# Kernel tuning notes

Hardware: AMD Instinct MI355X
Metric: run time of the kernel (lower is better)

## Reference

```python
import jax, jax.numpy as jnp
import numpy as np
import math

D = 128      # d_model == num_filters
L = 4        # num_conv_layers
K = 7        # kernel_size
H = 8        # num_heads
B, S = 64, 400


def setup_inputs() -> dict:
    key = jax.random.key(0)
    ks = jax.random.split(key, 24)
    s = 0.02
    inp = {}
    inp['x'] = jax.random.normal(ks[0], (B, S, D), dtype=jnp.float32)
    # per-conv-layer params (stacked over L)
    inp['ln_g'] = jnp.ones((L, D), jnp.float32)
    inp['ln_b'] = jnp.zeros((L, D), jnp.float32)
    inp['dw_w'] = jax.random.normal(ks[1], (L, D, D, K), dtype=jnp.float32) * s
    inp['dw_b'] = jnp.zeros((L, D), jnp.float32)
    inp['pw_w'] = jax.random.normal(ks[2], (L, D, D), dtype=jnp.float32) * s
    inp['pw_b'] = jnp.zeros((L, D), jnp.float32)
    # attention block
    inp['attln_g'] = jnp.ones((D,), jnp.float32)
    inp['attln_b'] = jnp.zeros((D,), jnp.float32)
    inp['wq'] = jax.random.normal(ks[3], (D, D), dtype=jnp.float32) * s
    inp['bq'] = jnp.zeros((D,), jnp.float32)
    inp['wk'] = jax.random.normal(ks[4], (D, D), dtype=jnp.float32) * s
    inp['bk'] = jnp.zeros((D,), jnp.float32)
    inp['wv'] = jax.random.normal(ks[5], (D, D), dtype=jnp.float32) * s
    inp['bv'] = jnp.zeros((D,), jnp.float32)
    inp['wp'] = jax.random.normal(ks[6], (D, D), dtype=jnp.float32) * s
    inp['bp'] = jnp.zeros((D,), jnp.float32)
    # ffn
    inp['ffnln_g'] = jnp.ones((D,), jnp.float32)
    inp['ffnln_b'] = jnp.zeros((D,), jnp.float32)
    inp['fc_w'] = jax.random.normal(ks[7], (D, D), dtype=jnp.float32) * s
    inp['fc_b'] = jnp.zeros((D,), jnp.float32)
    return inp


def _layernorm(x, g, b, eps=1e-5):
    mu = jnp.mean(x, axis=-1, keepdims=True)
    var = jnp.var(x, axis=-1, keepdims=True)
    return (x - mu) * jax.lax.rsqrt(var + eps) * g + b


def _pos_encoding(seq_len, channels, dtype):
    pos = jnp.arange(seq_len, dtype=dtype)                       # [S]
    freq = 1.0 / (10000.0 ** (jnp.arange(0, channels, 2, dtype=dtype) / channels))
    sin_inp = pos[:, None] * freq[None, :]                       # [S, C/2]
    return jnp.concatenate([jnp.sin(sin_inp), jnp.cos(sin_inp)], axis=-1)  # [S, C]


def _encoder_fwd(x, ln_g, ln_b, dw_w, dw_b, pw_w, pw_b,
                 attln_g, attln_b, wq, bq, wk, bk, wv, bv, wp, bp,
                 ffnln_g, ffnln_b, fc_w, fc_b):
    b, s, d = x.shape
    out = x + _pos_encoding(s, d, x.dtype)[None, :, :]

    # conv stack: LN -> transpose -> (full) conv K -> pointwise conv -> transpose
    pad = dw_w.shape[-1] // 2
    for i in range(dw_w.shape[0]):
        h = _layernorm(out, ln_g[i], ln_b[i])
        t = jnp.transpose(h, (0, 2, 1))                          # [B, D, S]
        t = jax.lax.conv_general_dilated(
            t, dw_w[i], window_strides=(1,), padding=[(pad, pad)],
            dimension_numbers=('NCH', 'OIH', 'NCH')) + dw_b[i][None, :, None]
        t = jnp.einsum('bds,fd->bfs', t, pw_w[i]) + pw_b[i][None, :, None]
        out = jnp.transpose(t, (0, 2, 1))                        # [B, S, D]

    # causal self-attention (explicit scores, per original)
    h = _layernorm(out, attln_g, attln_b)
    hd = d // H
    q = (jnp.einsum('bsd,od->bso', h, wq) + bq).reshape(b, s, H, hd)
    k = (jnp.einsum('bsd,od->bso', h, wk) + bk).reshape(b, s, H, hd)
    v = (jnp.einsum('bsd,od->bso', h, wv) + bv).reshape(b, s, H, hd)
    att = jnp.einsum('bqhd,bkhd->bhqk', q, k) / math.sqrt(hd)    # [B, H, S, S]
    causal = jnp.tril(jnp.ones((s, s), dtype=bool))
    att = jnp.where(causal[None, None], att, jnp.asarray(-1e10, att.dtype))
    att = jax.nn.softmax(att, axis=-1)
    y = jnp.einsum('bhqk,bkhd->bqhd', att, v).reshape(b, s, d)
    y = jnp.einsum('bsd,od->bso', y, wp) + bp

    # ffn
    y = _layernorm(y, ffnln_g, ffnln_b)
    y = jnp.einsum('bsd,od->bso', y, fc_w) + fc_b
    return jax.nn.relu(y)


def reference(x, ln_g, ln_b, dw_w, dw_b, pw_w, pw_b,
              attln_g, attln_b, wq, bq, wk, bk, wv, bv, wp, bp,
              ffnln_g, ffnln_b, fc_w, fc_b):
    return _encoder_fwd(x, ln_g, ln_b, dw_w, dw_b, pw_w, pw_b,
                        attln_g, attln_b, wq, bq, wk, bk, wv, bv, wp, bp,
                        ffnln_g, ffnln_b, fc_w, fc_b)
```

## Files before the change

### kernel.cpp

```cpp
#include <hip/hip_runtime.h>
#include <hip/hip_bf16.h>
#include <math.h>

#define Dm 128
#define Lc 4
#define Kc 7
#define Hh 8
#define Bb 64
#define Ss 400
#define SsP 416
#define TOK (Bb*Ss)

typedef __attribute__((ext_vector_type(8))) short bf16x8;
typedef __attribute__((ext_vector_type(4))) float f32x4;

__device__ __forceinline__ unsigned short f2bf(float f) {
    __hip_bfloat16 h = __float2bfloat16(f);
    return __builtin_bit_cast(unsigned short, h);
}
__device__ __forceinline__ unsigned int packbf(float a, float b) {
    return (unsigned int)f2bf(a) | ((unsigned int)f2bf(b) << 16);
}
__device__ __forceinline__ bf16x8 pack8(float4 a, float4 b) {
    unsigned int u0 = packbf(a.x, a.y), u1 = packbf(a.z, a.w);
    unsigned int u2 = packbf(b.x, b.y), u3 = packbf(b.z, b.w);
    uint4 u = make_uint4(u0, u1, u2, u3);
    return __builtin_bit_cast(bf16x8, u);
}


__global__ __launch_bounds__(256) void prep_misc(const float* __restrict__ wq, const float* __restrict__ wk,
                                                 const float* __restrict__ wv, const float* __restrict__ wp,
                                                 const float* __restrict__ fc,
                                                 const float* __restrict__ pw_w, const float* __restrict__ dw_b,
                                                 const float* __restrict__ pw_b,
                                                 float* __restrict__ pe, unsigned short* __restrict__ wf,
                                                 float* __restrict__ mb) {
    int blk = blockIdx.x;
    if (blk < 200) {
        int s = blk * 2 + (threadIdx.x >> 7);
        int c = threadIdx.x & 127;
        int j = (c < 64) ? c : (c - 64);
        float freq = expf(-(2.0f * j / 128.0f) * 9.210340371976184f);
        float a = (float)s * freq;
        pe[s * Dm + c] = (c < 64) ? sinf(a) : cosf(a);
    } else if (blk < 520) {
        int idx = (blk - 200) * 256 + threadIdx.x;
        int m = idx >> 14;
        int r = idx & 16383;
        int fragi = r >> 9, lr = (r >> 3) & 63, j = r & 7;
        int kb = fragi >> 3, nb = fragi & 7;
        int o = nb * 16 + (lr & 15);
        int d = kb * 32 + (lr >> 4) * 8 + j;
        const float* src = (m == 0) ? wq : (m == 1) ? wk : (m == 2) ? wv : (m == 3) ? wp : fc;
        wf[idx] = f2bf(src[o * Dm + d]);
    } else {
        int l = blk - 520;
        int f = threadIdx.x;
        if (f < Dm) {
            const float* pwl = pw_w + ((size_t)l * Dm + f) * Dm;
            const float* db  = dw_b + l * Dm;
            float acc = pw_b[l * Dm + f];
            #pragma unroll 8
            for (int c4 = 0; c4 < 32; ++c4) {
                float4 p = *(const float4*)(pwl + c4 * 4);
                float4 d = *(const float4*)(db + c4 * 4);
                acc += p.x * d.x + p.y * d.y + p.z * d.z + p.w * d.w;
            }
            mb[l * Dm + f] = acc;
        }
    }
}


__global__ __launch_bounds__(256) void merge_conv_mfma(const float* __restrict__ pw_w,
                                                       const float* __restrict__ dw_w,
                                                       unsigned short* __restrict__ mwf) {
    __shared__ unsigned short dwS[64][136];
    int blk = blockIdx.x;
    int ih = blk & 1;
    int k  = (blk >> 1) % 7;
    int l  = blk / 14;
    int tid = threadIdx.x, lane = tid & 63, w = tid >> 6;

    const float* dwl = dw_w + (size_t)l * (Dm * Dm * Kc) + k;
    for (int it = 0; it < 32; ++it) {
        int idx = it * 256 + tid;
        int c = idx >> 6, il = idx & 63;
        int i = ih * 64 + il;
        dwS[il][c] = f2bf(dwl[(size_t)(c * Dm + i) * Kc]);
    }
    __syncthreads();

    const float* pwl = pw_w + (size_t)l * Dm * Dm;
    int arow = lane & 15, ac = (lane >> 4) * 8;
    f32x4 acc[2][4];
    #pragma unroll
    for (int n = 0; n < 2; ++n)
        #pragma unroll
        for (int m = 0; m < 4; ++m) acc[n][m] = (f32x4){0.f, 0.f, 0.f, 0.f};

    #pragma unroll
    for (int kb = 0; kb < 4; ++kb) {
        int c0 = kb * 32 + ac;
        bf16x8 Bf[2];
        #pragma unroll
        for (int n = 0; n < 2; ++n) {
            int f = (w * 2 + n) * 16 + arow;
            const float* rp = pwl + (size_t)f * Dm + c0;
            Bf[n] = pack8(*(const float4*)rp, *(const float4*)(rp + 4));
        }
        #pragma unroll
        for (int m = 0; m < 4; ++m) {
            bf16x8 af = *(const bf16x8*)&dwS[m * 16 + arow][c0];
            acc[0][m] = __builtin_amdgcn_mfma_f32_16x16x32_bf16(af, Bf[0], acc[0][m], 0, 0, 0);
            acc[1][m] = __builtin_amdgcn_mfma_f32_16x16x32_bf16(af, Bf[1], acc[1][m], 0, 0, 0);
        }
    }
    #pragma unroll
    for (int n = 0; n < 2; ++n) {
        int nb = w * 2 + n;
        #pragma unroll
        for (int m = 0; m < 4; ++m) {
            int i0 = ih * 64 + m * 16 + (lane >> 4) * 4;
            int ib = i0 >> 5, i32 = i0 & 31;
            int lanep = ((i32 >> 3) << 4) | arow;
            int jb = i32 & 7;
            size_t frag = ((size_t)(l * 28 + (k * 4 + ib)) * 8 + nb);
            *(uint2*)(mwf + frag * 512 + lanep * 8 + jb) =
                make_uint2(packbf(acc[n][m][0], acc[n][m][1]),
                           packbf(acc[n][m][2], acc[n][m][3]));
        }
    }
}


__device__ __forceinline__ uint4 ln_pack(float4 v0, float4 v1,
                                         const float* __restrict__ g,
                                         const float* __restrict__ b, int c16) {
    float sum = v0.x + v0.y + v0.z + v0.w + v1.x + v1.y + v1.z + v1.w;
    float sq  = v0.x*v0.x + v0.y*v0.y + v0.z*v0.z + v0.w*v0.w
              + v1.x*v1.x + v1.y*v1.y + v1.z*v1.z + v1.w*v1.w;
    #pragma unroll
    for (int off = 8; off; off >>= 1) {
        sum += __shfl_xor(sum, off);
        sq  += __shfl_xor(sq, off);
    }
    float mu = sum * (1.0f / 128.0f);
    float var = sq * (1.0f / 128.0f) - mu * mu;
    float rs = rsqrtf(var + 1e-5f);
    float4 g0 = *(const float4*)(g + c16 * 8);
    float4 g1 = *(const float4*)(g + c16 * 8 + 4);
    float4 b0 = *(const float4*)(b + c16 * 8);
    float4 b1 = *(const float4*)(b + c16 * 8 + 4);
    uint4 o;
    o.x = packbf((v0.x - mu) * rs * g0.x + b0.x, (v0.y - mu) * rs * g0.y + b0.y);
    o.y = packbf((v0.z - mu) * rs * g0.z + b0.z, (v0.w - mu) * rs * g0.w + b0.w);
    o.z = packbf((v1.x - mu) * rs * g1.x + b1.x, (v1.y - mu) * rs * g1.y + b1.y);
    o.w = packbf((v1.z - mu) * rs * g1.z + b1.z, (v1.w - mu) * rs * g1.w + b1.w);
    return o;
}


__global__ __launch_bounds__(256) void conv_mfma(const float* __restrict__ in,
                                                 const float* __restrict__ pe,
                                                 const unsigned short* __restrict__ mwf,
                                                 const float* __restrict__ mb,
                                                 const float* __restrict__ lng,
                                                 const float* __restrict__ lnb,
                                                 float* __restrict__ out) {
    __shared__ unsigned short hs[54][136];
    int tid = threadIdx.x;
    int lane = tid & 63, w = tid >> 6;
    int bI = blockIdx.x / 9;
    int st = blockIdx.x % 9;
    int s0 = st * 48;
    const float* ib = in + (size_t)bI * Ss * Dm;
    for (int c = tid; c < 54 * 16; c += 256) {
        int row = c >> 4, c16 = c & 15;
        int gs = s0 - 3 + row;
        if (gs >= 0 && gs < Ss) {
            const float* rp = ib + (size_t)gs * Dm + c16 * 8;
            float4 v0 = *(const float4*)rp;
            float4 v1 = *(const float4*)(rp + 4);
            if (pe) {
                const float* pp = pe + (size_t)gs * Dm + c16 * 8;
                float4 p0 = *(const float4*)pp;
                float4 p1 = *(const float4*)(pp + 4);
                v0.x += p0.x; v0.y += p0.y; v0.z += p0.z; v0.w += p0.w;
                v1.x += p1.x; v1.y += p1.y; v1.z += p1.z; v1.w += p1.w;
            }
            *(uint4*)&hs[row][c16 * 8] = ln_pack(v0, v1, lng, lnb, c16);
        } else {
            *(uint4*)&hs[row][c16 * 8] = make_uint4(0u, 0u, 0u, 0u);
        }
    }
    __syncthreads();

    f32x4 acc[2][3];
    #pragma unroll
    for (int n = 0; n < 2; ++n)
        #pragma unroll
        for (int m = 0; m < 3; ++m) acc[n][m] = (f32x4){0.f, 0.f, 0.f, 0.f};

    int nb0 = w * 2;
    int arow = lane & 15, acol = (lane >> 4) * 8;
    #pragma unroll 4
    for (int kb = 0; kb < 28; ++kb) {
        int k = kb >> 2, i0 = (kb & 3) * 32;
        bf16x8 b0 = *(const bf16x8*)(mwf + ((size_t)(kb * 8 + nb0)) * 512 + lane * 8);
        bf16x8 b1 = *(const bf16x8*)(mwf + ((size_t)(kb * 8 + nb0 + 1)) * 512 + lane * 8);
        #pragma unroll
        for (int m = 0; m < 3; ++m) {
            bf16x8 af = *(const bf16x8*)&hs[m * 16 + arow + k][i0 + acol];
            acc[0][m] = __builtin_amdgcn_mfma_f32_16x16x32_bf16(af, b0, acc[0][m], 0, 0, 0);
            acc[1][m] = __builtin_amdgcn_mfma_f32_16x16x32_bf16(af, b1, acc[1][m], 0, 0, 0);
        }
    }
    int rr = (lane >> 4) * 4;
    #pragma unroll
    for (int n = 0; n < 2; ++n) {
        int f0 = (nb0 + n) * 16;
        float bias = mb[f0 + arow];
        #pragma unroll
        for (int m = 0; m < 3; ++m)
            #pragma unroll
            for (int r = 0; r < 4; ++r) {
                int s = s0 + m * 16 + rr + r;
                if (s < Ss)
                    out[((size_t)bI * Ss + s) * Dm + f0 + arow] = acc[n][m][r] + bias;
            }
    }
}


__global__ __launch_bounds__(256) void qkv_mfma(const float* __restrict__ in,
                                                const float* __restrict__ lng,
                                                const float* __restrict__ lnb,
                                                const unsigned short* __restrict__ wfb,
                                                const float* __restrict__ bq,
                                                const float* __restrict__ bk,
                                                const float* __restrict__ bv,
                                                unsigned short* __restrict__ Qo,
                                                unsigned short* __restrict__ Ko,
                                                unsigned short* __restrict__ Vo) {
    __shared__ unsigned short hs[80][136];
    int tid = threadIdx.x;
    int lane = tid & 63, w = tid >> 6;
    int mat = blockIdx.y;
    int bI = blockIdx.x / 5;
    int sb = (blockIdx.x % 5) * 80;
    const float* ib = in + ((size_t)bI * Ss + sb) * Dm;
    for (int c = tid; c < 80 * 16; c += 256) {
        int row = c >> 4, c16 = c & 15;
        const float* rp = ib + (size_t)row * Dm + c16 * 8;
        float4 v0 = *(const float4*)rp;
        float4 v1 = *(const float4*)(rp + 4);
        *(uint4*)&hs[row][c16 * 8] = ln_pack(v0, v1, lng, lnb, c16);
    }
    __syncthreads();

    const unsigned short* wf = wfb + (size_t)mat * 16384;
    f32x4 acc[2][5];
    #pragma unroll
    for (int n = 0; n < 2; ++n)
        #pragma unroll
        for (int m = 0; m < 5; ++m) acc[n][m] = (f32x4){0.f, 0.f, 0.f, 0.f};

    int nb0 = w * 2;
    int arow = lane & 15, acol = (lane >> 4) * 8;
    #pragma unroll
    for (int kb = 0; kb < 4; ++kb) {
        bf16x8 b0 = *(const bf16x8*)(wf + ((size_t)(kb * 8 + nb0)) * 512 + lane * 8);
        bf16x8 b1 = *(const bf16x8*)(wf + ((size_t)(kb * 8 + nb0 + 1)) * 512 + lane * 8);
        #pragma unroll
        for (int m = 0; m < 5; ++m) {
            bf16x8 af = *(const bf16x8*)&hs[m * 16 + arow][kb * 32 + acol];
            acc[0][m] = __builtin_amdgcn_mfma_f32_16x16x32_bf16(af, b0, acc[0][m], 0, 0, 0);
            acc[1][m] = __builtin_amdgcn_mfma_f32_16x16x32_bf16(af, b1, acc[1][m], 0, 0, 0);
        }
    }
    int rr = (lane >> 4) * 4;
    const float* bias = (mat == 0) ? bq : (mat == 1) ? bk : bv;
    float sc = (mat == 0) ? 0.25f : 1.0f;
    #pragma unroll
    for (int n = 0; n < 2; ++n) {
        int hI = nb0 + n;
        float bvv = bias[hI * 16 + arow];
        if (mat < 2) {
            unsigned short* qo = (mat == 0) ? Qo : Ko;
            #pragma unroll
            for (int m = 0; m < 5; ++m)
                #pragma unroll
                for (int r = 0; r < 4; ++r) {
                    int s = sb + m * 16 + rr + r;
                    qo[(((size_t)(bI * Hh + hI)) * Ss + s) * 16 + arow] = f2bf((acc[n][m][r] + bvv) * sc);
                }
        } else {
            unsigned short* base = Vo + ((size_t)(bI * Hh + hI) * 16 + arow) * SsP + sb;
            #pragma unroll
            for (int m = 0; m < 5; ++m) {
                unsigned lo = packbf(acc[n][m][0] + bvv, acc[n][m][1] + bvv);
                unsigned hi = packbf(acc[n][m][2] + bvv, acc[n][m][3] + bvv);
                *(uint2*)(base + m * 16 + rr) = make_uint2(lo, hi);
            }
        }
    }
}


__global__ __launch_bounds__(256) void gemm2(const void* __restrict__ inv,
                                             const unsigned short* __restrict__ wf,
                                             const float* __restrict__ bias,
                                             const float* __restrict__ lng,
                                             const float* __restrict__ lnb,
                                             float* __restrict__ out, int relu) {
    __shared__ unsigned short hs[80][136];
    int tid = threadIdx.x;
    int lane = tid & 63, w = tid >> 6;
    size_t tok0 = (size_t)blockIdx.x * 80;
    if (lng) {
        const float* ib = (const float*)inv + tok0 * Dm;
        for (int c = tid; c < 80 * 16; c += 256) {
            int row = c >> 4, c16 = c & 15;
            const float* rp = ib + (size_t)row * Dm + c16 * 8;
            float4 v0 = *(const float4*)rp;
            float4 v1 = *(const float4*)(rp + 4);
            *(uint4*)&hs[row][c16 * 8] = ln_pack(v0, v1, lng, lnb, c16);
        }
    } else {
        const unsigned short* ib = (const unsigned short*)inv + tok0 * Dm;
        for (int c = tid; c < 80 * 16; c += 256) {
            int row = c >> 4, c16 = c & 15;
            *(uint4*)&hs[row][c16 * 8] = *(const uint4*)(ib + (size_t)row * Dm + c16 * 8);
        }
    }
    __syncthreads();

    f32x4 acc[2][5];
    #pragma unroll
    for (int n = 0; n < 2; ++n)
        #pragma unroll
        for (int m = 0; m < 5; ++m) acc[n][m] = (f32x4){0.f, 0.f, 0.f, 0.f};

    int nb0 = w * 2;
    int arow = lane & 15, acol = (lane >> 4) * 8;
    #pragma unroll
    for (int kb = 0; kb < 4; ++kb) {
        bf16x8 b0 = *(const bf16x8*)(wf + ((size_t)(kb * 8 + nb0)) * 512 + lane * 8);
        bf16x8 b1 = *(const bf16x8*)(wf + ((size_t)(kb * 8 + nb0 + 1)) * 512 + lane * 8);
        #pragma unroll
        for (int m = 0; m < 5; ++m) {
            bf16x8 af = *(const bf16x8*)&hs[m * 16 + arow][kb * 32 + acol];
            acc[0][m] = __builtin_amdgcn_mfma_f32_16x16x32_bf16(af, b0, acc[0][m], 0, 0, 0);
            acc[1][m] = __builtin_amdgcn_mfma_f32_16x16x32_bf16(af, b1, acc[1][m], 0, 0, 0);
        }
    }
    int rr = (lane >> 4) * 4;
    #pragma unroll
    for (int n = 0; n < 2; ++n) {
        int f0 = (nb0 + n) * 16;
        float bvv = bias[f0 + arow];
        #pragma unroll
        for (int m = 0; m < 5; ++m)
            #pragma unroll
            for (int r = 0; r < 4; ++r) {
                float v = acc[n][m][r] + bvv;
                if (relu) v = fmaxf(v, 0.f);
                out[(tok0 + m * 16 + rr + r) * Dm + f0 + arow] = v;
            }
    }
}


__global__ __launch_bounds__(256) void attn_mfma(const unsigned short* __restrict__ Q,
                                                 const unsigned short* __restrict__ Kb,
                                                 const unsigned short* __restrict__ VT,
                                                 unsigned short* __restrict__ out) {
    int wid = threadIdx.x >> 6, lane = threadIdx.x & 63;
    int gw = blockIdx.x * 4 + wid;
    int bh = gw & 511, qt = gw >> 9;
    int q15 = lane & 15, h = lane >> 4;
    int qg = qt * 16 + q15;

    uint4 qv = make_uint4(0u, 0u, 0u, 0u);
    if (h < 2) qv = *(const uint4*)(Q + ((size_t)bh * Ss + qg) * 16 + h * 8);
    bf16x8 qf = __builtin_bit_cast(bf16x8, qv);

    f32x4 o = (f32x4){0.f, 0.f, 0.f, 0.f};
    float mrow = -1e30f, lrow = 0.f;
    const unsigned short* kbase = Kb + (size_t)bh * Ss * 16;
    const unsigned short* vbase = VT + ((size_t)bh * 16 + q15) * SsP;

    for (int kt = 0; kt <= qt; kt += 2) {
        int kg0 = kt * 16 + q15;
        uint4 k0 = make_uint4(0u, 0u, 0u, 0u), k1 = make_uint4(0u, 0u, 0u, 0u);
        if (h < 2) {
            k0 = *(const uint4*)(kbase + (size_t)kg0 * 16 + h * 8);
            if (kg0 + 16 < Ss)
                k1 = *(const uint4*)(kbase + (size_t)(kg0 + 16) * 16 + h * 8);
        }
        f32x4 z = (f32x4){0.f, 0.f, 0.f, 0.f};
        f32x4 s0 = __builtin_amdgcn_mfma_f32_16x16x32_bf16(__builtin_bit_cast(bf16x8, k0), qf, z, 0, 0, 0);
        f32x4 s1 = __builtin_amdgcn_mfma_f32_16x16x32_bf16(__builtin_bit_cast(bf16x8, k1), qf, z, 0, 0, 0);

        float p[8];
        #pragma unroll
        for (int r = 0; r < 4; ++r) {
            int ka = kt * 16 + h * 4 + r;
            p[r]     = (ka <= qg)      ? s0[r] : -1e30f;
            p[r + 4] = (ka + 16 <= qg) ? s1[r] : -1e30f;
        }
        float tm = fmaxf(fmaxf(fmaxf(p[0], p[1]), fmaxf(p[2], p[3])),
                         fmaxf(fmaxf(p[4], p[5]), fmaxf(p[6], p[7])));
        tm = fmaxf(tm, __shfl_xor(tm, 16));
        tm = fmaxf(tm, __shfl_xor(tm, 32));
        float mnew = fmaxf(mrow, tm);
        float corr = __expf(mrow - mnew);
        float psum = 0.f;
        #pragma unroll
        for (int r = 0; r < 8; ++r) { p[r] = __expf(p[r] - mnew); psum += p[r]; }
        psum += __shfl_xor(psum, 16);
        psum += __shfl_xor(psum, 32);
        lrow = lrow * corr + psum;
        mrow = mnew;
        o[0] *= corr; o[1] *= corr; o[2] *= corr; o[3] *= corr;

        unsigned pk0 = packbf(p[0], p[1]), pk1 = packbf(p[2], p[3]);
        unsigned pk2 = packbf(p[4], p[5]), pk3 = packbf(p[6], p[7]);
        int srcA = q15 + ((h & 1) << 5);
        int srcB = srcA + 16;
        unsigned a0 = __shfl(pk0, srcA), a1 = __shfl(pk1, srcA);
        unsigned a2 = __shfl(pk0, srcB), a3 = __shfl(pk1, srcB);
        unsigned b0 = __shfl(pk2, srcA), b1 = __shfl(pk3, srcA);
        unsigned b2 = __shfl(pk2, srcB), b3 = __shfl(pk3, srcB);
        bool t1 = h >= 2;
        uint4 pw = make_uint4(t1 ? b0 : a0, t1 ? b1 : a1, t1 ? b2 : a2, t1 ? b3 : a3);

        uint4 vv = *(const uint4*)(vbase + kt * 16 + h * 8);
        o = __builtin_amdgcn_mfma_f32_16x16x32_bf16(__builtin_bit_cast(bf16x8, vv),
                                                    __builtin_bit_cast(bf16x8, pw), o, 0, 0, 0);
    }
    float inv = 1.0f / lrow;
    int bI = bh >> 3, hh = bh & 7;
    unsigned short* op = out + ((size_t)bI * Ss + qg) * Dm + hh * 16 + h * 4;
    *(uint2*)op = make_uint2(packbf(o[0] * inv, o[1] * inv),
                             packbf(o[2] * inv, o[3] * inv));
}


extern "C" void kernel_launch(void* const* d_in, const int* in_sizes, int n_in,
                              void* d_out, int out_size, void* d_ws, size_t ws_size,
                              hipStream_t stream) {
    (void)in_sizes; (void)n_in; (void)out_size; (void)ws_size;
    const float* x       = (const float*)d_in[0];
    const float* ln_g    = (const float*)d_in[1];
    const float* ln_b    = (const float*)d_in[2];
    const float* dw_w    = (const float*)d_in[3];
    const float* dw_b    = (const float*)d_in[4];
    const float* pw_w    = (const float*)d_in[5];
    const float* pw_b    = (const float*)d_in[6];
    const float* attln_g = (const float*)d_in[7];
    const float* attln_b = (const float*)d_in[8];
    const float* wq = (const float*)d_in[9];
    const float* bq = (const float*)d_in[10];
    const float* wk = (const float*)d_in[11];
    const float* bk = (const float*)d_in[12];
    const float* wv = (const float*)d_in[13];
    const float* bv = (const float*)d_in[14];
    const float* wp = (const float*)d_in[15];
    const float* bp = (const float*)d_in[16];
    const float* ffnln_g = (const float*)d_in[17];
    const float* ffnln_b = (const float*)d_in[18];
    const float* fc_w = (const float*)d_in[19];
    const float* fc_b = (const float*)d_in[20];

    float* ws = (float*)d_ws;
    float* pe = ws;
    float* mb = pe + 51200;
    float* C1 = mb + 512;
    float* C2 = C1 + 3276800;
    unsigned short* mwf = (unsigned short*)(C2 + 3276800);
    unsigned short* wfb = mwf + 458752;
    unsigned short* Qb  = wfb + 81920;
    unsigned short* Kb2 = Qb + 3276800;
    unsigned short* VTb = Kb2 + 3276800;
    unsigned short* A1b = VTb + 3407872;

    prep_misc<<<524, 256, 0, stream>>>(wq, wk, wv, wp, fc_w, pw_w, dw_b, pw_b, pe, wfb, mb);
    merge_conv_mfma<<<56, 256, 0, stream>>>(pw_w, dw_w, mwf);

    conv_mfma<<<Bb * 9, 256, 0, stream>>>(x,  pe,      mwf,                    mb,           ln_g,           ln_b,           C1);
    conv_mfma<<<Bb * 9, 256, 0, stream>>>(C1, nullptr, mwf + 114688,           mb + Dm,      ln_g + Dm,      ln_b + Dm,      C2);
    conv_mfma<<<Bb * 9, 256, 0, stream>>>(C2, nullptr, mwf + 2 * 114688,       mb + 2 * Dm,  ln_g + 2 * Dm,  ln_b + 2 * Dm,  C1);
    conv_mfma<<<Bb * 9, 256, 0, stream>>>(C1, nullptr, mwf + 3 * 114688,       mb + 3 * Dm,  ln_g + 3 * Dm,  ln_b + 3 * Dm,  C2);

    qkv_mfma<<<dim3(320, 3), 256, 0, stream>>>(C2, attln_g, attln_b, wfb, bq, bk, bv, Qb, Kb2, VTb);
    attn_mfma<<<3200, 256, 0, stream>>>(Qb, Kb2, VTb, A1b);
    gemm2<<<320, 256, 0, stream>>>(A1b, wfb + 3 * 16384, bp, nullptr, nullptr, C1, 0);

    gemm2<<<320, 256, 0, stream>>>(C1, wfb + 4 * 16384, fc_b, ffnln_g, ffnln_b, (float*)d_out, 1);
}
```

Baseline: 130.1 us.

## Merge prep kernels, split-bf16 conv weight merge, fuse QK in qkv, widen attention tile

Folds the conv weight-merge kernel into the prep kernel so one launch does both. The merge now uses a hi/lo bf16 split with three MFMAs for better weight precision. qkv now runs two grid rows, with one block computing both Q and K to reuse the layernormed tile. The attention inner loop handles four key tiles per online-softmax step, with V padded to 448 so the extra reads stay in bounds. This cuts launches, reductions and rescale work per key, at the cost of more registers, extra merge MFMAs and fewer qkv blocks.

```diff
diff --git a/kernel.cpp b/kernel.cpp
--- a/kernel.cpp
+++ b/kernel.cpp
@@ -8,12 +8,15 @@
 #define Hh 8
 #define Bb 64
 #define Ss 400
-#define SsP 416
+#define SsP 448
 #define TOK (Bb*Ss)
 
 typedef __attribute__((ext_vector_type(8))) short bf16x8;
 typedef __attribute__((ext_vector_type(4))) float f32x4;
 
+__device__ __forceinline__ float bf2f(unsigned int u) {
+    union { unsigned int i; float f; } x; x.i = u << 16; return x.f;
+}
 __device__ __forceinline__ unsigned short f2bf(float f) {
     __hip_bfloat16 h = __float2bfloat16(f);
     return __builtin_bit_cast(unsigned short, h);
@@ -21,31 +24,30 @@
 __device__ __forceinline__ unsigned int packbf(float a, float b) {
     return (unsigned int)f2bf(a) | ((unsigned int)f2bf(b) << 16);
 }
-__device__ __forceinline__ bf16x8 pack8(float4 a, float4 b) {
-    unsigned int u0 = packbf(a.x, a.y), u1 = packbf(a.z, a.w);
-    unsigned int u2 = packbf(b.x, b.y), u3 = packbf(b.z, b.w);
-    uint4 u = make_uint4(u0, u1, u2, u3);
-    return __builtin_bit_cast(bf16x8, u);
-}
-
-
-__global__ __launch_bounds__(256) void prep_misc(const float* __restrict__ wq, const float* __restrict__ wk,
-                                                 const float* __restrict__ wv, const float* __restrict__ wp,
-                                                 const float* __restrict__ fc,
-                                                 const float* __restrict__ pw_w, const float* __restrict__ dw_b,
-                                                 const float* __restrict__ pw_b,
-                                                 float* __restrict__ pe, unsigned short* __restrict__ wf,
-                                                 float* __restrict__ mb) {
+
+
+__global__ __launch_bounds__(256) void prep_all(const float* __restrict__ wq, const float* __restrict__ wk,
+                                                const float* __restrict__ wv, const float* __restrict__ wp,
+                                                const float* __restrict__ fc,
+                                                const float* __restrict__ pw_w, const float* __restrict__ dw_w,
+                                                const float* __restrict__ dw_b, const float* __restrict__ pw_b,
+                                                float* __restrict__ pe, unsigned short* __restrict__ wf,
+                                                float* __restrict__ mb, unsigned short* __restrict__ mwf) {
+    __shared__ unsigned short hiS[64][136];
+    __shared__ unsigned short loS[64][136];
     int blk = blockIdx.x;
+    int tid = threadIdx.x;
     if (blk < 200) {
-        int s = blk * 2 + (threadIdx.x >> 7);
-        int c = threadIdx.x & 127;
+        int s = blk * 2 + (tid >> 7);
+        int c = tid & 127;
         int j = (c < 64) ? c : (c - 64);
         float freq = expf(-(2.0f * j / 128.0f) * 9.210340371976184f);
         float a = (float)s * freq;
         pe[s * Dm + c] = (c < 64) ? sinf(a) : cosf(a);
-    } else if (blk < 520) {
-        int idx = (blk - 200) * 256 + threadIdx.x;
+        return;
+    }
+    if (blk < 520) {
+        int idx = (blk - 200) * 256 + tid;
         int m = idx >> 14;
         int r = idx & 16383;
         int fragi = r >> 9, lr = (r >> 3) & 63, j = r & 7;
@@ -54,9 +56,11 @@
         int d = kb * 32 + (lr >> 4) * 8 + j;
         const float* src = (m == 0) ? wq : (m == 1) ? wk : (m == 2) ? wv : (m == 3) ? wp : fc;
         wf[idx] = f2bf(src[o * Dm + d]);
-    } else {
+        return;
+    }
+    if (blk < 524) {
         int l = blk - 520;
-        int f = threadIdx.x;
+        int f = tid;
         if (f < Dm) {
             const float* pwl = pw_w + ((size_t)l * Dm + f) * Dm;
             const float* db  = dw_b + l * Dm;
@@ -69,26 +73,24 @@
             }
             mb[l * Dm + f] = acc;
         }
-    }
-}
-
-
-__global__ __launch_bounds__(256) void merge_conv_mfma(const float* __restrict__ pw_w,
-                                                       const float* __restrict__ dw_w,
-                                                       unsigned short* __restrict__ mwf) {
-    __shared__ unsigned short dwS[64][136];
-    int blk = blockIdx.x;
-    int ih = blk & 1;
-    int k  = (blk >> 1) % 7;
-    int l  = blk / 14;
-    int tid = threadIdx.x, lane = tid & 63, w = tid >> 6;
+        return;
+    }
+    int mblk = blk - 524;
+    int ih = mblk & 1;
+    int k  = (mblk >> 1) % 7;
+    int l  = mblk / 14;
+    int lane = tid & 63, w = tid >> 6;
 
     const float* dwl = dw_w + (size_t)l * (Dm * Dm * Kc) + k;
     for (int it = 0; it < 32; ++it) {
         int idx = it * 256 + tid;
         int c = idx >> 6, il = idx & 63;
         int i = ih * 64 + il;
-        dwS[il][c] = f2bf(dwl[(size_t)(c * Dm + i) * Kc]);
+        float x = dwl[(size_t)(c * Dm + i) * Kc];
+        unsigned short hi = f2bf(x);
+        float lo = x - bf2f(hi);
+        hiS[il][c] = hi;
+        loS[il][c] = f2bf(lo);
     }
     __syncthreads();
 
@@ -103,18 +105,41 @@
     #pragma unroll
     for (int kb = 0; kb < 4; ++kb) {
         int c0 = kb * 32 + ac;
-        bf16x8 Bf[2];
+        bf16x8 Bhi[2], Blo[2];
         #pragma unroll
         for (int n = 0; n < 2; ++n) {
             int f = (w * 2 + n) * 16 + arow;
             const float* rp = pwl + (size_t)f * Dm + c0;
-            Bf[n] = pack8(*(const float4*)rp, *(const float4*)(rp + 4));
+            float4 a = *(const float4*)rp;
+            float4 b = *(const float4*)(rp + 4);
+            float v[8] = {a.x, a.y, a.z, a.w, b.x, b.y, b.z, b.w};
+            unsigned short hh[8], ll[8];
+            #pragma unroll
+            for (int j = 0; j < 8; ++j) {
+                hh[j] = f2bf(v[j]);
+                ll[j] = f2bf(v[j] - bf2f(hh[j]));
+            }
+            uint4 uh = make_uint4((unsigned)hh[0] | ((unsigned)hh[1] << 16),
+                                  (unsigned)hh[2] | ((unsigned)hh[3] << 16),
+                                  (unsigned)hh[4] | ((unsigned)hh[5] << 16),
+                                  (unsigned)hh[6] | ((unsigned)hh[7] << 16));
+            uint4 ul = make_uint4((unsigned)ll[0] | ((unsigned)ll[1] << 16),
+                                  (unsigned)ll[2] | ((unsigned)ll[3] << 16),
+                                  (unsigned)ll[4] | ((unsigned)ll[5] << 16),
+                                  (unsigned)ll[6] | ((unsigned)ll[7] << 16));
+            Bhi[n] = __builtin_bit_cast(bf16x8, uh);
+            Blo[n] = __builtin_bit_cast(bf16x8, ul);
         }
         #pragma unroll
         for (int m = 0; m < 4; ++m) {
-            bf16x8 af = *(const bf16x8*)&dwS[m * 16 + arow][c0];
-            acc[0][m] = __builtin_amdgcn_mfma_f32_16x16x32_bf16(af, Bf[0], acc[0][m], 0, 0, 0);
-            acc[1][m] = __builtin_amdgcn_mfma_f32_16x16x32_bf16(af, Bf[1], acc[1][m], 0, 0, 0);
+            bf16x8 ahi = *(const bf16x8*)&hiS[m * 16 + arow][c0];
+            bf16x8 alo = *(const bf16x8*)&loS[m * 16 + arow][c0];
+            #pragma unroll
+            for (int n = 0; n < 2; ++n) {
+                acc[n][m] = __builtin_amdgcn_mfma_f32_16x16x32_bf16(ahi, Bhi[n], acc[n][m], 0, 0, 0);
+                acc[n][m] = __builtin_amdgcn_mfma_f32_16x16x32_bf16(ahi, Blo[n], acc[n][m], 0, 0, 0);
+                acc[n][m] = __builtin_amdgcn_mfma_f32_16x16x32_bf16(alo, Bhi[n], acc[n][m], 0, 0, 0);
+            }
         }
     }
     #pragma unroll
@@ -247,7 +272,7 @@
     __shared__ unsigned short hs[80][136];
     int tid = threadIdx.x;
     int lane = tid & 63, w = tid >> 6;
-    int mat = blockIdx.y;
+    int y = blockIdx.y;
     int bI = blockIdx.x / 5;
     int sb = (blockIdx.x % 5) * 80;
     const float* ib = in + ((size_t)bI * Ss + sb) * Dm;
@@ -260,49 +285,52 @@
     }
     __syncthreads();
 
-    const unsigned short* wf = wfb + (size_t)mat * 16384;
-    f32x4 acc[2][5];
-    #pragma unroll
-    for (int n = 0; n < 2; ++n)
-        #pragma unroll
-        for (int m = 0; m < 5; ++m) acc[n][m] = (f32x4){0.f, 0.f, 0.f, 0.f};
-
     int nb0 = w * 2;
     int arow = lane & 15, acol = (lane >> 4) * 8;
-    #pragma unroll
-    for (int kb = 0; kb < 4; ++kb) {
-        bf16x8 b0 = *(const bf16x8*)(wf + ((size_t)(kb * 8 + nb0)) * 512 + lane * 8);
-        bf16x8 b1 = *(const bf16x8*)(wf + ((size_t)(kb * 8 + nb0 + 1)) * 512 + lane * 8);
-        #pragma unroll
-        for (int m = 0; m < 5; ++m) {
-            bf16x8 af = *(const bf16x8*)&hs[m * 16 + arow][kb * 32 + acol];
-            acc[0][m] = __builtin_amdgcn_mfma_f32_16x16x32_bf16(af, b0, acc[0][m], 0, 0, 0);
-            acc[1][m] = __builtin_amdgcn_mfma_f32_16x16x32_bf16(af, b1, acc[1][m], 0, 0, 0);
-        }
-    }
-    int rr = (lane >> 4) * 4;
-    const float* bias = (mat == 0) ? bq : (mat == 1) ? bk : bv;
-    float sc = (mat == 0) ? 0.25f : 1.0f;
-    #pragma unroll
-    for (int n = 0; n < 2; ++n) {
-        int hI = nb0 + n;
-        float bvv = bias[hI * 16 + arow];
-        if (mat < 2) {
-            unsigned short* qo = (mat == 0) ? Qo : Ko;
-            #pragma unroll
-            for (int m = 0; m < 5; ++m)
+    int nmat = (y == 0) ? 2 : 1;
+    for (int mi = 0; mi < nmat; ++mi) {
+        int mat = (y == 0) ? mi : 2;
+        const unsigned short* wf = wfb + (size_t)mat * 16384;
+        f32x4 acc[2][5];
+        #pragma unroll
+        for (int n = 0; n < 2; ++n)
+            #pragma unroll
+            for (int m = 0; m < 5; ++m) acc[n][m] = (f32x4){0.f, 0.f, 0.f, 0.f};
+        #pragma unroll
+        for (int kb = 0; kb < 4; ++kb) {
+            bf16x8 b0 = *(const bf16x8*)(wf + ((size_t)(kb * 8 + nb0)) * 512 + lane * 8);
+            bf16x8 b1 = *(const bf16x8*)(wf + ((size_t)(kb * 8 + nb0 + 1)) * 512 + lane * 8);
+            #pragma unroll
+            for (int m = 0; m < 5; ++m) {
+                bf16x8 af = *(const bf16x8*)&hs[m * 16 + arow][kb * 32 + acol];
+                acc[0][m] = __builtin_amdgcn_mfma_f32_16x16x32_bf16(af, b0, acc[0][m], 0, 0, 0);
+                acc[1][m] = __builtin_amdgcn_mfma_f32_16x16x32_bf16(af, b1, acc[1][m], 0, 0, 0);
+            }
+        }
+        int rr = (lane >> 4) * 4;
+        const float* bias = (mat == 0) ? bq : (mat == 1) ? bk : bv;
+        float sc = (mat == 0) ? 0.25f : 1.0f;
+        #pragma unroll
+        for (int n = 0; n < 2; ++n) {
+            int hI = nb0 + n;
+            float bvv = bias[hI * 16 + arow];
+            if (mat < 2) {
+                unsigned short* qo = (mat == 0) ? Qo : Ko;
                 #pragma unroll
-                for (int r = 0; r < 4; ++r) {
-                    int s = sb + m * 16 + rr + r;
-                    qo[(((size_t)(bI * Hh + hI)) * Ss + s) * 16 + arow] = f2bf((acc[n][m][r] + bvv) * sc);
+                for (int m = 0; m < 5; ++m)
+                    #pragma unroll
+                    for (int r = 0; r < 4; ++r) {
+                        int s = sb + m * 16 + rr + r;
+                        qo[(((size_t)(bI * Hh + hI)) * Ss + s) * 16 + arow] = f2bf((acc[n][m][r] + bvv) * sc);
+                    }
+            } else {
+                unsigned short* base = Vo + ((size_t)(bI * Hh + hI) * 16 + arow) * SsP + sb;
+                #pragma unroll
+                for (int m = 0; m < 5; ++m) {
+                    unsigned lo = packbf(acc[n][m][0] + bvv, acc[n][m][1] + bvv);
+                    unsigned hi = packbf(acc[n][m][2] + bvv, acc[n][m][3] + bvv);
+                    *(uint2*)(base + m * 16 + rr) = make_uint2(lo, hi);
                 }
-        } else {
-            unsigned short* base = Vo + ((size_t)(bI * Hh + hI) * 16 + arow) * SsP + sb;
-            #pragma unroll
-            for (int m = 0; m < 5; ++m) {
-                unsigned lo = packbf(acc[n][m][0] + bvv, acc[n][m][1] + bvv);
-                unsigned hi = packbf(acc[n][m][2] + bvv, acc[n][m][3] + bvv);
-                *(uint2*)(base + m * 16 + rr) = make_uint2(lo, hi);
             }
         }
     }
@@ -391,55 +419,62 @@
     float mrow = -1e30f, lrow = 0.f;
     const unsigned short* kbase = Kb + (size_t)bh * Ss * 16;
     const unsigned short* vbase = VT + ((size_t)bh * 16 + q15) * SsP;
-
-    for (int kt = 0; kt <= qt; kt += 2) {
-        int kg0 = kt * 16 + q15;
-        uint4 k0 = make_uint4(0u, 0u, 0u, 0u), k1 = make_uint4(0u, 0u, 0u, 0u);
-        if (h < 2) {
-            k0 = *(const uint4*)(kbase + (size_t)kg0 * 16 + h * 8);
-            if (kg0 + 16 < Ss)
-                k1 = *(const uint4*)(kbase + (size_t)(kg0 + 16) * 16 + h * 8);
-        }
-        f32x4 z = (f32x4){0.f, 0.f, 0.f, 0.f};
-        f32x4 s0 = __builtin_amdgcn_mfma_f32_16x16x32_bf16(__builtin_bit_cast(bf16x8, k0), qf, z, 0, 0, 0);
-        f32x4 s1 = __builtin_amdgcn_mfma_f32_16x16x32_bf16(__builtin_bit_cast(bf16x8, k1), qf, z, 0, 0, 0);
-
-        float p[8];
-        #pragma unroll
-        for (int r = 0; r < 4; ++r) {
-            int ka = kt * 16 + h * 4 + r;
-            p[r]     = (ka <= qg)      ? s0[r] : -1e30f;
-            p[r + 4] = (ka + 16 <= qg) ? s1[r] : -1e30f;
-        }
-        float tm = fmaxf(fmaxf(fmaxf(p[0], p[1]), fmaxf(p[2], p[3])),
-                         fmaxf(fmaxf(p[4], p[5]), fmaxf(p[6], p[7])));
+    int srcA = q15 + ((h & 1) << 5);
+    int srcB = srcA + 16;
+    bool t1 = h >= 2;
+    f32x4 z = (f32x4){0.f, 0.f, 0.f, 0.f};
+
+    for (int kt0 = 0; kt0 <= qt; kt0 += 4) {
+        uint4 kv[4];
+        #pragma unroll
+        for (int t = 0; t < 4; ++t) {
+            kv[t] = make_uint4(0u, 0u, 0u, 0u);
+            if (h < 2 && kt0 + t <= qt)
+                kv[t] = *(const uint4*)(kbase + (size_t)((kt0 + t) * 16 + q15) * 16 + h * 8);
+        }
+        f32x4 s[4];
+        #pragma unroll
+        for (int t = 0; t < 4; ++t)
+            s[t] = __builtin_amdgcn_mfma_f32_16x16x32_bf16(__builtin_bit_cast(bf16x8, kv[t]), qf, z, 0, 0, 0);
+
+        float p[16];
+        #pragma unroll
+        for (int t = 0; t < 4; ++t)
+            #pragma unroll
+            for (int r = 0; r < 4; ++r) {
+                int ka = (kt0 + t) * 16 + h * 4 + r;
+                p[t * 4 + r] = (ka <= qg) ? s[t][r] : -1e30f;
+            }
+        float tm = p[0];
+        #pragma unroll
+        for (int i = 1; i < 16; ++i) tm = fmaxf(tm, p[i]);
         tm = fmaxf(tm, __shfl_xor(tm, 16));
         tm = fmaxf(tm, __shfl_xor(tm, 32));
         float mnew = fmaxf(mrow, tm);
         float corr = __expf(mrow - mnew);
         float psum = 0.f;
         #pragma unroll
-        for (int r = 0; r < 8; ++r) { p[r] = __expf(p[r] - mnew); psum += p[r]; }
+        for (int i = 0; i < 16; ++i) { p[i] = __expf(p[i] - mnew); psum += p[i]; }
         psum += __shfl_xor(psum, 16);
         psum += __shfl_xor(psum, 32);
         lrow = lrow * corr + psum;
         mrow = mnew;
         o[0] *= corr; o[1] *= corr; o[2] *= corr; o[3] *= corr;
 
-        unsigned pk0 = packbf(p[0], p[1]), pk1 = packbf(p[2], p[3]);
-        unsigned pk2 = packbf(p[4], p[5]), pk3 = packbf(p[6], p[7]);
-        int srcA = q15 + ((h & 1) << 5);
-        int srcB = srcA + 16;
-        unsigned a0 = __shfl(pk0, srcA), a1 = __shfl(pk1, srcA);
-        unsigned a2 = __shfl(pk0, srcB), a3 = __shfl(pk1, srcB);
-        unsigned b0 = __shfl(pk2, srcA), b1 = __shfl(pk3, srcA);
-        unsigned b2 = __shfl(pk2, srcB), b3 = __shfl(pk3, srcB);
-        bool t1 = h >= 2;
-        uint4 pw = make_uint4(t1 ? b0 : a0, t1 ? b1 : a1, t1 ? b2 : a2, t1 ? b3 : a3);
-
-        uint4 vv = *(const uint4*)(vbase + kt * 16 + h * 8);
-        o = __builtin_amdgcn_mfma_f32_16x16x32_bf16(__builtin_bit_cast(bf16x8, vv),
-                                                    __builtin_bit_cast(bf16x8, pw), o, 0, 0, 0);
+        #pragma unroll
+        for (int pr = 0; pr < 2; ++pr) {
+            const float* pp = p + pr * 8;
+            unsigned pk0 = packbf(pp[0], pp[1]), pk1 = packbf(pp[2], pp[3]);
+            unsigned pk2 = packbf(pp[4], pp[5]), pk3 = packbf(pp[6], pp[7]);
+            unsigned a0 = __shfl(pk0, srcA), a1 = __shfl(pk1, srcA);
+            unsigned a2 = __shfl(pk0, srcB), a3 = __shfl(pk1, srcB);
+            unsigned b0 = __shfl(pk2, srcA), b1 = __shfl(pk3, srcA);
+            unsigned b2 = __shfl(pk2, srcB), b3 = __shfl(pk3, srcB);
+            uint4 pw = make_uint4(t1 ? b0 : a0, t1 ? b1 : a1, t1 ? b2 : a2, t1 ? b3 : a3);
+            uint4 vv = *(const uint4*)(vbase + (kt0 + pr * 2) * 16 + h * 8);
+            o = __builtin_amdgcn_mfma_f32_16x16x32_bf16(__builtin_bit_cast(bf16x8, vv),
+                                                        __builtin_bit_cast(bf16x8, pw), o, 0, 0, 0);
+        }
     }
     float inv = 1.0f / lrow;
     int bI = bh >> 3, hh = bh & 7;
@@ -485,17 +520,17 @@
     unsigned short* Qb  = wfb + 81920;
     unsigned short* Kb2 = Qb + 3276800;
     unsigned short* VTb = Kb2 + 3276800;
-    unsigned short* A1b = VTb + 3407872;
-
-    prep_misc<<<524, 256, 0, stream>>>(wq, wk, wv, wp, fc_w, pw_w, dw_b, pw_b, pe, wfb, mb);
-    merge_conv_mfma<<<56, 256, 0, stream>>>(pw_w, dw_w, mwf);
+    unsigned short* A1b = VTb + 3670016;
+
+    prep_all<<<580, 256, 0, stream>>>(wq, wk, wv, wp, fc_w, pw_w, dw_w, dw_b, pw_b,
+                                      pe, wfb, mb, mwf);
 
     conv_mfma<<<Bb * 9, 256, 0, stream>>>(x,  pe,      mwf,                    mb,           ln_g,           ln_b,           C1);
     conv_mfma<<<Bb * 9, 256, 0, stream>>>(C1, nullptr, mwf + 114688,           mb + Dm,      ln_g + Dm,      ln_b + Dm,      C2);
     conv_mfma<<<Bb * 9, 256, 0, stream>>>(C2, nullptr, mwf + 2 * 114688,       mb + 2 * Dm,  ln_g + 2 * Dm,  ln_b + 2 * Dm,  C1);
     conv_mfma<<<Bb * 9, 256, 0, stream>>>(C1, nullptr, mwf + 3 * 114688,       mb + 3 * Dm,  ln_g + 3 * Dm,  ln_b + 3 * Dm,  C2);
 
-    qkv_mfma<<<dim3(320, 3), 256, 0, stream>>>(C2, attln_g, attln_b, wfb, bq, bk, bv, Qb, Kb2, VTb);
+    qkv_mfma<<<dim3(320, 2), 256, 0, stream>>>(C2, attln_g, attln_b, wfb, bq, bk, bv, Qb, Kb2, VTb);
     attn_mfma<<<3200, 256, 0, stream>>>(Qb, Kb2, VTb, A1b);
     gemm2<<<320, 256, 0, stream>>>(A1b, wfb + 3 * 16384, bp, nullptr, nullptr, C1, 0);
 
```

New measurement: 128.4 us. No clear change (-1.3%).
